# Optimization experiments

Hardware: AMD Instinct MI355X
Metric: run time of the kernel (lower is better)

The kernel has to match this reference:

```python
import jax, jax.numpy as jnp
import numpy as np

NUM_LAYERS = 6
KS = 5  # kernel_size; also attention window size K
EPS_IN = 1e-5  # torch InstanceNorm1d default eps


def _conv1d(x, w, b, d, p):
    # x: [N,C,L], w: [O,I,KS], dilated 'same' conv
    y = jax.lax.conv_general_dilated(x, w, window_strides=(1,), padding=[(p, p)],
                                     rhs_dilation=(d,), dimension_numbers=('NCH', 'OIH', 'NCH'))
    return y + b[None, :, None]


def _pw(x, w, b):
    # pointwise (1x1) conv: x [N,C,L], w [O,C]
    return jnp.einsum('oc,ncl->nol', w, x) + b[None, :, None]


def _layer(x, x_cross, pr, d):
    C, L = x.shape[1], x.shape[2]
    p = (KS // 2) * d  # padding
    conv_w, conv_b, qw, qb, kw, kb, vw, vb, f1w, f1b, f2w, f2b = pr
    out1 = _conv1d(x, conv_w, conv_b, d, p)
    xc = jnp.concatenate([x, x_cross], axis=1)
    q = _pw(xc, qw, qb)            # [N,C,L]
    k = _pw(xc, kw, kb)
    v = _pw(x, vw, vb)
    kp = jnp.pad(k, ((0, 0), (0, 0), (p, p)))
    vp = jnp.pad(v, ((0, 0), (0, 0), (p, p)))
    # attn index for query q, slot j is (q + j*d) into padded axis -> shifted slices
    win_k = jnp.stack([kp[:, :, j * d:j * d + L] for j in range(KS)], axis=-1)  # [N,C,L,K]
    win_v = jnp.stack([vp[:, :, j * d:j * d + L] for j in range(KS)], axis=-1)
    att = jnp.einsum('ncl,nclk->nlk', q, win_k) / np.float32(np.sqrt(C))
    pos = jnp.arange(L)[:, None] + (jnp.arange(KS)[None, :] - KS // 2) * d  # absolute key pos
    mask = (pos >= 0) & (pos < L)  # [L,K]
    att = jax.nn.softmax(att + jnp.log(mask + 1e-6), axis=-1) * mask
    r = jnp.einsum('nlk,nclk->ncl', att, win_v)
    h = out1 + r
    # InstanceNorm1d (no affine): normalize over L per (n,c)
    mu = jnp.mean(h, axis=2, keepdims=True)
    var = jnp.var(h, axis=2, keepdims=True)
    h = (h - mu) * jax.lax.rsqrt(var + EPS_IN)
    out = _pw(jax.nn.relu(_pw(h, f1w, f1b)), f2w, f2b)
    return x + out


def reference(x, x_cross, time_emb, time_w, time_b, conv_w, conv_b, qw, qb, kw, kb, vw, vb, f1w, f1b, f2w, f2b):
    te = time_emb * jax.nn.sigmoid(time_emb)  # swish
    x = x + (te @ time_w.T + time_b)[:, :, None]
    for i in range(NUM_LAYERS):
        pr = (conv_w[i], conv_b[i], qw[i], qb[i], kw[i], kb[i], vw[i], vb[i],
              f1w[i], f1b[i], f2w[i], f2b[i])
        x = _layer(x, x_cross, pr, 2 ** i)
    return x


def setup_inputs() -> dict:
    N, C, CC, L, T, nL = 4, 256, 256, 4096, 512, NUM_LAYERS
    key = jax.random.key(0)
    ks = jax.random.split(key, 18)
    s = 0.05
    return {
        'x': jax.random.normal(ks[0], (N, C, L), jnp.float32),
        'x_cross': jax.random.normal(ks[1], (N, CC, L), jnp.float32),
        'time_emb': jax.random.normal(ks[2], (N, T), jnp.float32),
        'time_w': jax.random.normal(ks[3], (C, T), jnp.float32) * s,
        'time_b': jax.random.normal(ks[4], (C,), jnp.float32) * s,
        'conv_w': jax.random.normal(ks[5], (nL, C, C, KS), jnp.float32) * s,
        'conv_b': jax.random.normal(ks[6], (nL, C), jnp.float32) * s,
        'qw': jax.random.normal(ks[7], (nL, C, C + CC), jnp.float32) * s,
        'qb': jax.random.normal(ks[8], (nL, C), jnp.float32) * s,
        'kw': jax.random.normal(ks[9], (nL, C, C + CC), jnp.float32) * s,
        'kb': jax.random.normal(ks[10], (nL, C), jnp.float32) * s,
        'vw': jax.random.normal(ks[11], (nL, C, C), jnp.float32) * s,
        'vb': jax.random.normal(ks[12], (nL, C), jnp.float32) * s,
        'f1w': jax.random.normal(ks[13], (nL, C, C), jnp.float32) * s,
        'f1b': jax.random.normal(ks[14], (nL, C), jnp.float32) * s,
        'f2w': jax.random.normal(ks[15], (nL, C, C), jnp.float32) * s,
        'f2b': jax.random.normal(ks[16], (nL, C), jnp.float32) * s,
    }
```

## Files before the change

### kernel.cpp

```cpp
#include <hip/hip_runtime.h>
#include <hip/hip_bf16.h>
#include <cstddef>
#include <cstdint>

#define N_   4
#define C_   256
#define L_   4096
#define T_   512
#define KS_  5
#define NL_  6
#define HALO 64
#define LP_  (L_ + 2 * HALO)
#define XCS  512
#define NCH  256

typedef __attribute__((ext_vector_type(8))) __bf16 bf16x8;
typedef __attribute__((ext_vector_type(4))) float f32x4;

#define VM_WAIT3 asm volatile("s_waitcnt vmcnt(3)" ::: "memory")
#define VM_WAIT2 asm volatile("s_waitcnt vmcnt(2)" ::: "memory")
#define VM_WAIT0 asm volatile("s_waitcnt vmcnt(0)" ::: "memory")

__device__ __forceinline__ void gload_lds16(const void* g, void* l) {
    __builtin_amdgcn_global_load_lds(
        (const __attribute__((address_space(1))) unsigned int*)g,
        (__attribute__((address_space(3))) unsigned int*)l, 16, 0, 0);
}
__device__ __forceinline__ float bf2f(unsigned short u) {
    union { unsigned int i; float f; } x; x.i = ((unsigned int)u) << 16; return x.f;
}
__device__ __forceinline__ unsigned short f2bf(float f) {
    __hip_bfloat16 h = __float2bfloat16(f);
    return *reinterpret_cast<unsigned short*>(&h);
}
__device__ __forceinline__ float4 ld4bf(const unsigned short* p) {
    ushort4 u = *reinterpret_cast<const ushort4*>(p);
    return make_float4(bf2f(u.x), bf2f(u.y), bf2f(u.z), bf2f(u.w));
}
__device__ __forceinline__ int swz(int row, int seg) { return seg ^ ((row >> 1) & 3); }

__device__ __forceinline__ void mfma16(bf16x8 af[4], bf16x8 bfr[4], f32x4 acc[4][4])
{
    #pragma unroll
    for (int m = 0; m < 4; m++)
        #pragma unroll
        for (int nn = 0; nn < 4; nn++)
            acc[m][nn] = __builtin_amdgcn_mfma_f32_16x16x32_bf16(af[m], bfr[nn], acc[m][nn], 0, 0, 0);
}

__global__ __launch_bounds__(512) void gemm_cq(
    const unsigned short* __restrict__ xcat,
    const unsigned short* __restrict__ wqkv, const float* __restrict__ qkvbias,
    const unsigned short* __restrict__ wconv, const float* __restrict__ cbias,
    unsigned short* __restrict__ qkvb, unsigned short* __restrict__ convb, int d)
{
    __shared__ alignas(16) unsigned short As[3][256 * 32];
    __shared__ alignas(16) unsigned short Bs[3][128 * 32];
    const int tid = threadIdx.x, wid = tid >> 6, lane = tid & 63;
    const int wr = wid >> 1, wc = wid & 1;
    const int r0 = blockIdx.x * 256;
    const int n = r0 >> 12, lb = r0 & (L_ - 1);
    const int ob = blockIdx.y;
    const bool isconv = (ob < 2);
    f32x4 acc[4][4] = {};
    const int orow = (lane >> 4) * 4, ocol = lane & 15;
    const int rsel = lane & 15, j = lane >> 4;

    auto read_frags = [&](const unsigned short* A, const unsigned short* B,
                          bf16x8 af[4], bf16x8 bfr[4]) {
        #pragma unroll
        for (int m = 0; m < 4; m++) {
            const int r = wr * 64 + m * 16 + rsel;
            af[m] = *reinterpret_cast<const bf16x8*>(&A[r * 32 + swz(r, j) * 8]);
        }
        #pragma unroll
        for (int nn = 0; nn < 4; nn++) {
            const int r = wc * 64 + nn * 16 + rsel;
            bfr[nn] = *reinterpret_cast<const bf16x8*>(&B[r * 32 + swz(r, j) * 8]);
        }
    };

    if (isconv) {
        const int o0 = ob * 128;
        auto stage = [&](int t, int b) {
            const int tap = t >> 3, kb = (t & 7) * 32;
            const size_t abase = (size_t)((long)n * LP_ + HALO + lb + (tap - 2) * d) * XCS;
            const unsigned short* Wj = wconv + (size_t)tap * C_ * C_;
            #pragma unroll
            for (int i = 0; i < 2; i++) {
                const int s = tid + i * 512, row = s >> 2, seg = s & 3;
                gload_lds16(xcat + abase + (size_t)row * XCS + kb + swz(row, seg) * 8,
                            As[b] + s * 8);
            }
            {
                const int row = tid >> 2, seg = tid & 3;
                gload_lds16(Wj + (size_t)(o0 + row) * C_ + kb + swz(row, seg) * 8,
                            Bs[b] + tid * 8);
            }
        };
        const int NT = 40;
        stage(0, 0); stage(1, 1);
        VM_WAIT3;
        __builtin_amdgcn_s_barrier();
        for (int t = 0; t < NT; t++) {
            const int cur = t % 3;
            bf16x8 af[4], bfr[4];
            read_frags(As[cur], Bs[cur], af, bfr);
            if (t + 2 < NT) stage(t + 2, (t + 2) % 3);
            mfma16(af, bfr, acc);
            if (t + 2 < NT) { VM_WAIT3; } else { VM_WAIT0; }
            __builtin_amdgcn_s_barrier();
        }
        #pragma unroll
        for (int m = 0; m < 4; m++)
            #pragma unroll
            for (int nn = 0; nn < 4; nn++) {
                const int gr0 = r0 + wr * 64 + m * 16 + orow;
                const int gc = o0 + wc * 64 + nn * 16 + ocol;
                const float bv = cbias[gc];
                #pragma unroll
                for (int rr = 0; rr < 4; rr++)
                    convb[(size_t)(gr0 + rr) * C_ + gc] = f2bf(acc[m][nn][rr] + bv);
            }
    } else {
        const int o0 = (ob - 2) * 128;
        const size_t abase = ((size_t)n * LP_ + HALO + lb) * XCS;
        auto stage = [&](int t, int b) {
            const int kb = t * 32;
            #pragma unroll
            for (int i = 0; i < 2; i++) {
                const int s = tid + i * 512, row = s >> 2, seg = s & 3;
                gload_lds16(xcat + abase + (size_t)row * XCS + kb + swz(row, seg) * 8,
                            As[b] + s * 8);
            }
            {
                const int row = tid >> 2, seg = tid & 3;
                gload_lds16(wqkv + (size_t)(o0 + row) * 512 + kb + swz(row, seg) * 8,
                            Bs[b] + tid * 8);
            }
        };
        const int NT = (o0 >= 512) ? 8 : 16;
        stage(0, 0); stage(1, 1);
        VM_WAIT3;
        __builtin_amdgcn_s_barrier();
        for (int t = 0; t < NT; t++) {
            const int cur = t % 3;
            bf16x8 af[4], bfr[4];
            read_frags(As[cur], Bs[cur], af, bfr);
            if (t + 2 < NT) stage(t + 2, (t + 2) % 3);
            mfma16(af, bfr, acc);
            if (t + 2 < NT) { VM_WAIT3; } else { VM_WAIT0; }
            __builtin_amdgcn_s_barrier();
        }
        #pragma unroll
        for (int m = 0; m < 4; m++)
            #pragma unroll
            for (int nn = 0; nn < 4; nn++) {
                const int gr0 = r0 + wr * 64 + m * 16 + orow;
                const int gc = o0 + wc * 64 + nn * 16 + ocol;
                const float bv = qkvbias[gc];
                #pragma unroll
                for (int rr = 0; rr < 4; rr++)
                    qkvb[(size_t)(gr0 + rr) * 768 + gc] = f2bf(acc[m][nn][rr] + bv);
            }
    }
}

template <int EP, int PERN>
__global__ __launch_bounds__(256) void gemm_f(
    const unsigned short* __restrict__ A,
    const unsigned short* __restrict__ B,
    const float* __restrict__ bias,
    unsigned short* __restrict__ outb,
    unsigned short* __restrict__ xcat)
{
    __shared__ alignas(16) unsigned short As[3][64 * 32];
    __shared__ alignas(16) unsigned short Bs[3][64 * 32];
    const int tid = threadIdx.x, wid = tid >> 6, lane = tid & 63;
    const int r0 = blockIdx.x * 64;
    const int o0 = blockIdx.y * 64;
    const int n = r0 >> 12;
    if (PERN) {
        B += (size_t)n * C_ * C_;
        bias += n * C_;
    }
    const size_t abase = (size_t)r0 * C_;
    const int rsel = lane & 15, j = lane >> 4;
    f32x4 acc[4] = {};
    auto stage = [&](int t, int b) {
        const int kb = t * 32;
        const int row = tid >> 2, seg = tid & 3;
        const int gso = swz(row, seg) * 8;
        gload_lds16(A + abase + (size_t)row * C_ + kb + gso, As[b] + tid * 8);
        gload_lds16(B + (size_t)(o0 + row) * C_ + kb + gso, Bs[b] + tid * 8);
    };
    const int NT = 8;
    stage(0, 0); stage(1, 1);
    VM_WAIT2;
    __builtin_amdgcn_s_barrier();
    for (int t = 0; t < NT; t++) {
        const int cur = t % 3;
        bf16x8 af, bfr[4];
        {
            const int r = wid * 16 + rsel;
            af = *reinterpret_cast<const bf16x8*>(&As[cur][r * 32 + swz(r, j) * 8]);
        }
        #pragma unroll
        for (int nn = 0; nn < 4; nn++) {
            const int r = nn * 16 + rsel;
            bfr[nn] = *reinterpret_cast<const bf16x8*>(&Bs[cur][r * 32 + swz(r, j) * 8]);
        }
        if (t + 2 < NT) stage(t + 2, (t + 2) % 3);
        #pragma unroll
        for (int nn = 0; nn < 4; nn++)
            acc[nn] = __builtin_amdgcn_mfma_f32_16x16x32_bf16(af, bfr[nn], acc[nn], 0, 0, 0);
        if (t + 2 < NT) { VM_WAIT2; } else { VM_WAIT0; }
        __builtin_amdgcn_s_barrier();
    }
    const int orow = (lane >> 4) * 4, ocol = lane & 15;
    #pragma unroll
    for (int nn = 0; nn < 4; nn++) {
        const int gr0 = r0 + wid * 16 + orow;
        const int gc = o0 + nn * 16 + ocol;
        const float bv = bias[gc];
        #pragma unroll
        for (int rr = 0; rr < 4; rr++) {
            const int gr = gr0 + rr;
            const float v = acc[nn][rr] + bv;
            if (EP == 2) {
                outb[(size_t)gr * C_ + gc] = f2bf(fmaxf(v, 0.f));
            } else {
                const int n2 = gr >> 12, ll = gr & (L_ - 1);
                unsigned short* xp = xcat + ((size_t)n2 * LP_ + HALO + ll) * XCS + gc;
                *xp = f2bf(v + bf2f(*xp));
            }
        }
    }
}

__global__ __launch_bounds__(256) void attn_fused(
    const unsigned short* __restrict__ qkv, const unsigned short* __restrict__ convb,
    unsigned short* __restrict__ hb2, float* __restrict__ psum, float* __restrict__ psq, int d)
{
    __shared__ float ps[4][256], pq[4][256];
    const int n = blockIdx.y;
    const int wave = threadIdx.x >> 6;
    const int lane = threadIdx.x & 63;
    float acs[4] = {0.f, 0.f, 0.f, 0.f}, acq[4] = {0.f, 0.f, 0.f, 0.f};
    for (int lq = 0; lq < 4; lq++) {
        const int l = blockIdx.x * 16 + wave * 4 + lq;
        const float4 qv = ld4bf(qkv + ((size_t)n * L_ + l) * 768 + lane * 4);
        float att[KS_];
        #pragma unroll
        for (int j = 0; j < KS_; j++) {
            const int lp = l + (j - 2) * d;
            float s = 0.f;
            if (lp >= 0 && lp < L_) {
                const float4 kv = ld4bf(qkv + ((size_t)n * L_ + lp) * 768 + 256 + lane * 4);
                s = qv.x * kv.x + qv.y * kv.y + qv.z * kv.z + qv.w * kv.w;
            }
            #pragma unroll
            for (int off = 32; off > 0; off >>= 1) s += __shfl_xor(s, off, 64);
            att[j] = s * 0.0625f;
        }
        float logit[KS_], m = -1e30f;
        #pragma unroll
        for (int j = 0; j < KS_; j++) {
            const int lp = l + (j - 2) * d;
            logit[j] = att[j] + logf(((lp >= 0 && lp < L_) ? 1.f : 0.f) + 1e-6f);
            m = fmaxf(m, logit[j]);
        }
        float den = 0.f, wgt[KS_];
        #pragma unroll
        for (int j = 0; j < KS_; j++) { wgt[j] = expf(logit[j] - m); den += wgt[j]; }
        const float inv = 1.f / den;
        float4 r = {0.f, 0.f, 0.f, 0.f};
        #pragma unroll
        for (int j = 0; j < KS_; j++) {
            const int lp = l + (j - 2) * d;
            if (lp < 0 || lp >= L_) continue;
            const float wj = wgt[j] * inv;
            const float4 vv = ld4bf(qkv + ((size_t)n * L_ + lp) * 768 + 512 + lane * 4);
            r.x += wj * vv.x; r.y += wj * vv.y; r.z += wj * vv.z; r.w += wj * vv.w;
        }
        const size_t rowoff = ((size_t)n * L_ + l) * C_ + lane * 4;
        const float4 cv = ld4bf(convb + rowoff);
        const float h0 = cv.x + r.x, h1 = cv.y + r.y, h2 = cv.z + r.z, h3 = cv.w + r.w;
        ushort4 ho;
        ho.x = f2bf(h0); ho.y = f2bf(h1); ho.z = f2bf(h2); ho.w = f2bf(h3);
        *(ushort4*)(hb2 + rowoff) = ho;
        acs[0] += h0; acs[1] += h1; acs[2] += h2; acs[3] += h3;
        acq[0] += h0 * h0; acq[1] += h1 * h1; acq[2] += h2 * h2; acq[3] += h3 * h3;
    }
    const int cb4 = lane * 4;
    #pragma unroll
    for (int u = 0; u < 4; u++) { ps[wave][cb4 + u] = acs[u]; pq[wave][cb4 + u] = acq[u]; }
    __syncthreads();
    const int t = threadIdx.x;
    psum[((size_t)n * NCH + blockIdx.x) * C_ + t] = ps[0][t] + ps[1][t] + ps[2][t] + ps[3][t];
    psq[((size_t)n * NCH + blockIdx.x) * C_ + t] = pq[0][t] + pq[1][t] + pq[2][t] + pq[3][t];
}

__global__ __launch_bounds__(256) void norm_red(
    const float* __restrict__ psum, const float* __restrict__ psq,
    float* __restrict__ psum2, float* __restrict__ psq2)
{
    const int g = blockIdx.x, n = blockIdx.y, c = threadIdx.x;
    float s = 0.f, ss = 0.f;
    for (int ch = g * 16; ch < g * 16 + 16; ch++) {
        s += psum[((size_t)n * NCH + ch) * C_ + c];
        ss += psq[((size_t)n * NCH + ch) * C_ + c];
    }
    psum2[((size_t)n * 16 + g) * C_ + c] = s;
    psq2[((size_t)n * 16 + g) * C_ + c] = ss;
}

__global__ __launch_bounds__(256) void fold_f1(
    const float* __restrict__ f1w, const float* __restrict__ f1b,
    const float* __restrict__ psum2, const float* __restrict__ psq2,
    unsigned short* __restrict__ W1p, float* __restrict__ b1eff)
{
    const int b = blockIdx.x;
    const int n = b >> 8, o = b & 255;
    const int c = threadIdx.x;
    const int lane = c & 63, wid = c >> 6;
    float s = 0.f, ss = 0.f;
    #pragma unroll
    for (int g = 0; g < 16; g++) {
        s += psum2[((size_t)n * 16 + g) * C_ + c];
        ss += psq2[((size_t)n * 16 + g) * C_ + c];
    }
    const float mu = s * (1.f / L_);
    const float scv = rsqrtf(ss * (1.f / L_) - mu * mu + 1e-5f);
    const float w = f1w[o * C_ + c];
    W1p[((size_t)n * C_ + o) * C_ + c] = f2bf(w * scv);
    float part = w * mu * scv;
    #pragma unroll
    for (int off = 32; off > 0; off >>= 1) part += __shfl_xor(part, off, 64);
    __shared__ float red[4];
    if (lane == 0) red[wid] = part;
    __syncthreads();
    if (c == 0) b1eff[n * C_ + o] = f1b[o] - (red[0] + red[1] + red[2] + red[3]);
}

__global__ __launch_bounds__(128) void time_bias_kernel(
    const float* __restrict__ te, const float* __restrict__ tw,
    const float* __restrict__ tb, float* __restrict__ bias)
{
    int nc = blockIdx.x;
    int n = nc >> 8, c = nc & 255;
    int tid = threadIdx.x;
    float s = 0.f;
    for (int t = tid; t < T_; t += 128) {
        float e = te[n * T_ + t];
        s += (e / (1.f + expf(-e))) * tw[c * T_ + t];
    }
    __shared__ float red[128];
    red[tid] = s;
    __syncthreads();
    for (int off = 64; off > 0; off >>= 1) {
        if (tid < off) red[tid] += red[tid + off];
        __syncthreads();
    }
    if (tid == 0) bias[nc] = red[0] + tb[c];
}

__global__ __launch_bounds__(256) void halo_zero(unsigned short* __restrict__ xcat)
{
    const int t = blockIdx.x * 256 + threadIdx.x;
    const int n = t >> 14, rr = (t >> 7) & 127, c4 = t & 127;
    const int row = (rr < 64) ? rr : (L_ + HALO) + (rr - 64);
    ushort4 z = {0, 0, 0, 0};
    *(ushort4*)(xcat + ((size_t)n * LP_ + row) * XCS + c4 * 4) = z;
}

template <int MODE>
__global__ __launch_bounds__(256) void transpose_in(
    const float* __restrict__ in, const float* __restrict__ bias,
    unsigned short* __restrict__ xcat)
{
    __shared__ float tile[32][33];
    const int n = blockIdx.z;
    const int l0 = blockIdx.x * 32, c0 = blockIdx.y * 32;
    const int tx = threadIdx.x, ty = threadIdx.y;
    #pragma unroll
    for (int i = 0; i < 4; i++) {
        int c = c0 + ty + 8 * i;
        tile[ty + 8 * i][tx] = in[((size_t)n * C_ + c) * L_ + l0 + tx];
    }
    __syncthreads();
    #pragma unroll
    for (int i = 0; i < 4; i++) {
        const int l = l0 + ty + 8 * i;
        const int c = c0 + tx;
        float v = tile[tx][ty + 8 * i];
        if (MODE == 0) {
            v += bias[n * C_ + c];
            xcat[((size_t)n * LP_ + HALO + l) * XCS + c] = f2bf(v);
        } else {
            xcat[((size_t)n * LP_ + HALO + l) * XCS + C_ + c] = f2bf(v);
        }
    }
}

__global__ __launch_bounds__(256) void transpose_out(
    const unsigned short* __restrict__ xcat, float* __restrict__ out)
{
    __shared__ float tile[32][33];
    const int n = blockIdx.z;
    const int l0 = blockIdx.x * 32, c0 = blockIdx.y * 32;
    const int tx = threadIdx.x, ty = threadIdx.y;
    #pragma unroll
    for (int i = 0; i < 4; i++) {
        int l = l0 + ty + 8 * i;
        tile[ty + 8 * i][tx] = bf2f(xcat[((size_t)n * LP_ + HALO + l) * XCS + c0 + tx]);
    }
    __syncthreads();
    #pragma unroll
    for (int i = 0; i < 4; i++) {
        int c = c0 + ty + 8 * i;
        out[((size_t)n * C_ + c) * L_ + l0 + tx] = tile[tx][ty + 8 * i];
    }
}

__global__ __launch_bounds__(256) void prep_qkv(
    const float* __restrict__ qw, const float* __restrict__ kw, const float* __restrict__ vw,
    const float* __restrict__ qb, const float* __restrict__ kb, const float* __restrict__ vb,
    unsigned short* __restrict__ W, float* __restrict__ Bias)
{
    const size_t idx = (size_t)blockIdx.x * 256 + threadIdx.x;
    const int layer = (int)(idx / (768 * 512));
    const int rem = (int)(idx % (768 * 512));
    const int row = rem >> 9, k = rem & 511;
    float v;
    if (row < 256) v = qw[((size_t)layer * 256 + row) * 512 + k];
    else if (row < 512) v = kw[((size_t)layer * 256 + row - 256) * 512 + k];
    else v = (k < 256) ? vw[((size_t)layer * 256 + row - 512) * 256 + k] : 0.f;
    W[idx] = f2bf(v);
    if (k == 0) {
        float b;
        if (row < 256) b = qb[layer * 256 + row];
        else if (row < 512) b = kb[layer * 256 + row - 256];
        else b = vb[layer * 256 + row - 512];
        Bias[layer * 768 + row] = b;
    }
}

__global__ __launch_bounds__(256) void prep_conv(
    const float* __restrict__ cw, unsigned short* __restrict__ W)
{
    const size_t idx = (size_t)blockIdx.x * 256 + threadIdx.x;
    const int layer = (int)(idx / (KS_ * C_ * C_));
    const int rem = (int)(idx % (KS_ * C_ * C_));
    const int j = rem / (C_ * C_);
    const int o = (rem / C_) & 255, c = rem & 255;
    W[idx] = f2bf(cw[(((size_t)layer * C_ + o) * C_ + c) * KS_ + j]);
}

__global__ __launch_bounds__(256) void conv_f2bf(
    const float* __restrict__ in, unsigned short* __restrict__ out, int nelem)
{
    const int idx = blockIdx.x * 256 + threadIdx.x;
    if (idx < nelem) out[idx] = f2bf(in[idx]);
}

extern "C" void kernel_launch(void* const* d_in, const int* in_sizes, int n_in,
                              void* d_out, int out_size, void* d_ws, size_t ws_size,
                              hipStream_t stream)
{
    (void)in_sizes; (void)n_in; (void)out_size; (void)ws_size;
    const float* x   = (const float*)d_in[0];
    const float* xc  = (const float*)d_in[1];
    const float* te  = (const float*)d_in[2];
    const float* tw  = (const float*)d_in[3];
    const float* tb  = (const float*)d_in[4];
    const float* cw  = (const float*)d_in[5];
    const float* cb  = (const float*)d_in[6];
    const float* qw  = (const float*)d_in[7];
    const float* qbi = (const float*)d_in[8];
    const float* kw  = (const float*)d_in[9];
    const float* kbi = (const float*)d_in[10];
    const float* vw  = (const float*)d_in[11];
    const float* vbi = (const float*)d_in[12];
    const float* f1w = (const float*)d_in[13];
    const float* f1b = (const float*)d_in[14];
    const float* f2w = (const float*)d_in[15];
    const float* f2b = (const float*)d_in[16];

    char* p = (char*)d_ws;
    auto alloc = [&](size_t bytes) { char* r = p; p += (bytes + 255) & ~(size_t)255; return r; };
    const size_t NLC = (size_t)N_ * L_ * C_;
    unsigned short* xcat  = (unsigned short*)alloc((size_t)N_ * LP_ * XCS * 2);
    unsigned short* qkvb  = (unsigned short*)alloc((size_t)N_ * L_ * 768 * 2);
    unsigned short* convb = (unsigned short*)alloc(NLC * 2);
    unsigned short* hb2   = (unsigned short*)alloc(NLC * 2);
    unsigned short* f1ob  = (unsigned short*)alloc(NLC * 2);
    unsigned short* wqkvb = (unsigned short*)alloc((size_t)NL_ * 768 * 512 * 2);
    unsigned short* wconvb= (unsigned short*)alloc((size_t)NL_ * KS_ * C_ * C_ * 2);
    unsigned short* wf2b  = (unsigned short*)alloc((size_t)NL_ * C_ * C_ * 2);
    unsigned short* W1p   = (unsigned short*)alloc((size_t)N_ * C_ * C_ * 2);
    float* b1eff  = (float*)alloc((size_t)N_ * C_ * 4);
    float* qkvbias = (float*)alloc((size_t)NL_ * 768 * 4);
    float* biasb = (float*)alloc(N_ * C_ * 4);
    float* psum  = (float*)alloc((size_t)N_ * NCH * C_ * 4);
    float* psq   = (float*)alloc((size_t)N_ * NCH * C_ * 4);
    float* psum2 = (float*)alloc((size_t)N_ * 16 * C_ * 4);
    float* psq2  = (float*)alloc((size_t)N_ * 16 * C_ * 4);

    halo_zero<<<256, 256, 0, stream>>>(xcat);
    prep_qkv<<<(NL_ * 768 * 512) / 256, 256, 0, stream>>>(qw, kw, vw, qbi, kbi, vbi, wqkvb, qkvbias);
    prep_conv<<<(NL_ * KS_ * C_ * C_) / 256, 256, 0, stream>>>(cw, wconvb);
    conv_f2bf<<<(NL_ * C_ * C_) / 256, 256, 0, stream>>>(f2w, wf2b, NL_ * C_ * C_);

    time_bias_kernel<<<N_ * C_, 128, 0, stream>>>(te, tw, tb, biasb);
    dim3 tgrid(L_ / 32, C_ / 32, N_), tblk(32, 8);
    transpose_in<0><<<tgrid, tblk, 0, stream>>>(x, biasb, xcat);
    transpose_in<1><<<tgrid, tblk, 0, stream>>>(xc, nullptr, xcat);

    for (int i = 0; i < NL_; i++) {
        const int d = 1 << i;
        gemm_cq<<<dim3(64, 8), 512, 0, stream>>>(
            xcat, wqkvb + (size_t)i * 768 * 512, qkvbias + i * 768,
            wconvb + (size_t)i * KS_ * C_ * C_, cb + i * C_, qkvb, convb, d);
        attn_fused<<<dim3(L_ / 16, N_), 256, 0, stream>>>(qkvb, convb, hb2, psum, psq, d);
        norm_red<<<dim3(16, N_), 256, 0, stream>>>(psum, psq, psum2, psq2);
        fold_f1<<<N_ * C_, 256, 0, stream>>>(
            f1w + (size_t)i * C_ * C_, f1b + i * C_, psum2, psq2, W1p, b1eff);
        gemm_f<2, 1><<<dim3(256, 4), 256, 0, stream>>>(
            hb2, W1p, b1eff, f1ob, nullptr);
        gemm_f<3, 0><<<dim3(256, 4), 256, 0, stream>>>(
            f1ob, wf2b + (size_t)i * C_ * C_, f2b + i * C_, nullptr, xcat);
    }
    transpose_out<<<tgrid, tblk, 0, stream>>>(xcat, (float*)d_out);
}
```

Measured before the change: 476.3 us.

## Recast dilated conv as per-tap pointwise GEMM columns summed in attention

Packs the five conv taps as extra output columns of a single unified GEMM with Q/K/V, so every GEMM block runs the same short K loop over unshifted rows. The attention kernel then gathers and sums the tap outputs at the dilated neighbor positions, alongside K and V, and adds the conv bias. This removes the long 40-step conv blocks and their load imbalance, but writes and rereads a much wider intermediate buffer per layer.

After: 497.2 us. 1.04x slower.

```diff
diff --git a/kernel.cpp b/kernel.cpp
--- a/kernel.cpp
+++ b/kernel.cpp
@@ -12,6 +12,7 @@
 #define HALO 64
 #define LP_  (L_ + 2 * HALO)
 #define XCS  512
+#define OBS  2048
 #define NCH  256
 
 typedef __attribute__((ext_vector_type(8))) __bf16 bf16x8;
@@ -48,11 +49,10 @@
             acc[m][nn] = __builtin_amdgcn_mfma_f32_16x16x32_bf16(af[m], bfr[nn], acc[m][nn], 0, 0, 0);
 }
 
-__global__ __launch_bounds__(512) void gemm_cq(
+__global__ __launch_bounds__(512) void gemm_all(
     const unsigned short* __restrict__ xcat,
-    const unsigned short* __restrict__ wqkv, const float* __restrict__ qkvbias,
-    const unsigned short* __restrict__ wconv, const float* __restrict__ cbias,
-    unsigned short* __restrict__ qkvb, unsigned short* __restrict__ convb, int d)
+    const unsigned short* __restrict__ wpack, const float* __restrict__ pbias,
+    unsigned short* __restrict__ obuf)
 {
     __shared__ alignas(16) unsigned short As[3][256 * 32];
     __shared__ alignas(16) unsigned short Bs[3][128 * 32];
@@ -60,110 +60,59 @@
     const int wr = wid >> 1, wc = wid & 1;
     const int r0 = blockIdx.x * 256;
     const int n = r0 >> 12, lb = r0 & (L_ - 1);
-    const int ob = blockIdx.y;
-    const bool isconv = (ob < 2);
+    const int o0 = blockIdx.y * 128;
+    const int NT = (blockIdx.y < 4) ? 16 : 8;
+    const size_t abase = ((size_t)n * LP_ + HALO + lb) * XCS;
     f32x4 acc[4][4] = {};
     const int orow = (lane >> 4) * 4, ocol = lane & 15;
     const int rsel = lane & 15, j = lane >> 4;
 
-    auto read_frags = [&](const unsigned short* A, const unsigned short* B,
-                          bf16x8 af[4], bf16x8 bfr[4]) {
+    auto stage = [&](int t, int b) {
+        const int kb = t * 32;
+        #pragma unroll
+        for (int i = 0; i < 2; i++) {
+            const int s = tid + i * 512, row = s >> 2, seg = s & 3;
+            gload_lds16(xcat + abase + (size_t)row * XCS + kb + swz(row, seg) * 8,
+                        As[b] + s * 8);
+        }
+        {
+            const int row = tid >> 2, seg = tid & 3;
+            gload_lds16(wpack + (size_t)(o0 + row) * 512 + kb + swz(row, seg) * 8,
+                        Bs[b] + tid * 8);
+        }
+    };
+    stage(0, 0); stage(1, 1);
+    VM_WAIT3;
+    __builtin_amdgcn_s_barrier();
+    for (int t = 0; t < NT; t++) {
+        const int cur = t % 3;
+        bf16x8 af[4], bfr[4];
         #pragma unroll
         for (int m = 0; m < 4; m++) {
             const int r = wr * 64 + m * 16 + rsel;
-            af[m] = *reinterpret_cast<const bf16x8*>(&A[r * 32 + swz(r, j) * 8]);
+            af[m] = *reinterpret_cast<const bf16x8*>(&As[cur][r * 32 + swz(r, j) * 8]);
         }
         #pragma unroll
         for (int nn = 0; nn < 4; nn++) {
             const int r = wc * 64 + nn * 16 + rsel;
-            bfr[nn] = *reinterpret_cast<const bf16x8*>(&B[r * 32 + swz(r, j) * 8]);
-        }
-    };
-
-    if (isconv) {
-        const int o0 = ob * 128;
-        auto stage = [&](int t, int b) {
-            const int tap = t >> 3, kb = (t & 7) * 32;
-            const size_t abase = (size_t)((long)n * LP_ + HALO + lb + (tap - 2) * d) * XCS;
-            const unsigned short* Wj = wconv + (size_t)tap * C_ * C_;
+            bfr[nn] = *reinterpret_cast<const bf16x8*>(&Bs[cur][r * 32 + swz(r, j) * 8]);
+        }
+        if (t + 2 < NT) stage(t + 2, (t + 2) % 3);
+        mfma16(af, bfr, acc);
+        if (t + 2 < NT) { VM_WAIT3; } else { VM_WAIT0; }
+        __builtin_amdgcn_s_barrier();
+    }
+    #pragma unroll
+    for (int m = 0; m < 4; m++)
+        #pragma unroll
+        for (int nn = 0; nn < 4; nn++) {
+            const int gr0 = r0 + wr * 64 + m * 16 + orow;
+            const int gc = o0 + wc * 64 + nn * 16 + ocol;
+            const float bv = pbias[gc];
             #pragma unroll
-            for (int i = 0; i < 2; i++) {
-                const int s = tid + i * 512, row = s >> 2, seg = s & 3;
-                gload_lds16(xcat + abase + (size_t)row * XCS + kb + swz(row, seg) * 8,
-                            As[b] + s * 8);
-            }
-            {
-                const int row = tid >> 2, seg = tid & 3;
-                gload_lds16(Wj + (size_t)(o0 + row) * C_ + kb + swz(row, seg) * 8,
-                            Bs[b] + tid * 8);
-            }
-        };
-        const int NT = 40;
-        stage(0, 0); stage(1, 1);
-        VM_WAIT3;
-        __builtin_amdgcn_s_barrier();
-        for (int t = 0; t < NT; t++) {
-            const int cur = t % 3;
-            bf16x8 af[4], bfr[4];
-            read_frags(As[cur], Bs[cur], af, bfr);
-            if (t + 2 < NT) stage(t + 2, (t + 2) % 3);
-            mfma16(af, bfr, acc);
-            if (t + 2 < NT) { VM_WAIT3; } else { VM_WAIT0; }
-            __builtin_amdgcn_s_barrier();
-        }
-        #pragma unroll
-        for (int m = 0; m < 4; m++)
-            #pragma unroll
-            for (int nn = 0; nn < 4; nn++) {
-                const int gr0 = r0 + wr * 64 + m * 16 + orow;
-                const int gc = o0 + wc * 64 + nn * 16 + ocol;
-                const float bv = cbias[gc];
-                #pragma unroll
-                for (int rr = 0; rr < 4; rr++)
-                    convb[(size_t)(gr0 + rr) * C_ + gc] = f2bf(acc[m][nn][rr] + bv);
-            }
-    } else {
-        const int o0 = (ob - 2) * 128;
-        const size_t abase = ((size_t)n * LP_ + HALO + lb) * XCS;
-        auto stage = [&](int t, int b) {
-            const int kb = t * 32;
-            #pragma unroll
-            for (int i = 0; i < 2; i++) {
-                const int s = tid + i * 512, row = s >> 2, seg = s & 3;
-                gload_lds16(xcat + abase + (size_t)row * XCS + kb + swz(row, seg) * 8,
-                            As[b] + s * 8);
-            }
-            {
-                const int row = tid >> 2, seg = tid & 3;
-                gload_lds16(wqkv + (size_t)(o0 + row) * 512 + kb + swz(row, seg) * 8,
-                            Bs[b] + tid * 8);
-            }
-        };
-        const int NT = (o0 >= 512) ? 8 : 16;
-        stage(0, 0); stage(1, 1);
-        VM_WAIT3;
-        __builtin_amdgcn_s_barrier();
-        for (int t = 0; t < NT; t++) {
-            const int cur = t % 3;
-            bf16x8 af[4], bfr[4];
-            read_frags(As[cur], Bs[cur], af, bfr);
-            if (t + 2 < NT) stage(t + 2, (t + 2) % 3);
-            mfma16(af, bfr, acc);
-            if (t + 2 < NT) { VM_WAIT3; } else { VM_WAIT0; }
-            __builtin_amdgcn_s_barrier();
-        }
-        #pragma unroll
-        for (int m = 0; m < 4; m++)
-            #pragma unroll
-            for (int nn = 0; nn < 4; nn++) {
-                const int gr0 = r0 + wr * 64 + m * 16 + orow;
-                const int gc = o0 + wc * 64 + nn * 16 + ocol;
-                const float bv = qkvbias[gc];
-                #pragma unroll
-                for (int rr = 0; rr < 4; rr++)
-                    qkvb[(size_t)(gr0 + rr) * 768 + gc] = f2bf(acc[m][nn][rr] + bv);
-            }
-    }
+            for (int rr = 0; rr < 4; rr++)
+                obuf[(size_t)(gr0 + rr) * OBS + gc] = f2bf(acc[m][nn][rr] + bv);
+        }
 }
 
 template <int EP, int PERN>
@@ -239,25 +188,31 @@
 }
 
 __global__ __launch_bounds__(256) void attn_fused(
-    const unsigned short* __restrict__ qkv, const unsigned short* __restrict__ convb,
+    const unsigned short* __restrict__ obuf, const float* __restrict__ cbias,
     unsigned short* __restrict__ hb2, float* __restrict__ psum, float* __restrict__ psq, int d)
 {
     __shared__ float ps[4][256], pq[4][256];
     const int n = blockIdx.y;
     const int wave = threadIdx.x >> 6;
     const int lane = threadIdx.x & 63;
+    const float4 cb = *(const float4*)(cbias + lane * 4);
     float acs[4] = {0.f, 0.f, 0.f, 0.f}, acq[4] = {0.f, 0.f, 0.f, 0.f};
     for (int lq = 0; lq < 4; lq++) {
         const int l = blockIdx.x * 16 + wave * 4 + lq;
-        const float4 qv = ld4bf(qkv + ((size_t)n * L_ + l) * 768 + lane * 4);
+        const size_t rb = ((size_t)n * L_ + l) * OBS;
+        const float4 qv = ld4bf(obuf + rb + lane * 4);
         float att[KS_];
+        float4 cv = {0.f, 0.f, 0.f, 0.f};
         #pragma unroll
         for (int j = 0; j < KS_; j++) {
             const int lp = l + (j - 2) * d;
             float s = 0.f;
             if (lp >= 0 && lp < L_) {
-                const float4 kv = ld4bf(qkv + ((size_t)n * L_ + lp) * 768 + 256 + lane * 4);
+                const size_t rp = ((size_t)n * L_ + lp) * OBS;
+                const float4 kv = ld4bf(obuf + rp + 256 + lane * 4);
                 s = qv.x * kv.x + qv.y * kv.y + qv.z * kv.z + qv.w * kv.w;
+                const float4 tv = ld4bf(obuf + rp + 768 + j * 256 + lane * 4);
+                cv.x += tv.x; cv.y += tv.y; cv.z += tv.z; cv.w += tv.w;
             }
             #pragma unroll
             for (int off = 32; off > 0; off >>= 1) s += __shfl_xor(s, off, 64);
@@ -280,12 +235,12 @@
             const int lp = l + (j - 2) * d;
             if (lp < 0 || lp >= L_) continue;
             const float wj = wgt[j] * inv;
-            const float4 vv = ld4bf(qkv + ((size_t)n * L_ + lp) * 768 + 512 + lane * 4);
+            const float4 vv = ld4bf(obuf + ((size_t)n * L_ + lp) * OBS + 512 + lane * 4);
             r.x += wj * vv.x; r.y += wj * vv.y; r.z += wj * vv.z; r.w += wj * vv.w;
         }
+        const float h0 = cv.x + cb.x + r.x, h1 = cv.y + cb.y + r.y;
+        const float h2 = cv.z + cb.z + r.z, h3 = cv.w + cb.w + r.w;
         const size_t rowoff = ((size_t)n * L_ + l) * C_ + lane * 4;
-        const float4 cv = ld4bf(convb + rowoff);
-        const float h0 = cv.x + r.x, h1 = cv.y + r.y, h2 = cv.z + r.z, h3 = cv.w + r.w;
         ushort4 ho;
         ho.x = f2bf(h0); ho.y = f2bf(h1); ho.z = f2bf(h2); ho.w = f2bf(h3);
         *(ushort4*)(hb2 + rowoff) = ho;
@@ -423,38 +378,32 @@
     }
 }
 
-__global__ __launch_bounds__(256) void prep_qkv(
-    const float* __restrict__ qw, const float* __restrict__ kw, const float* __restrict__ vw,
+__global__ __launch_bounds__(256) void prep_pack(
+    const float* __restrict__ qw, const float* __restrict__ kw,
+    const float* __restrict__ vw, const float* __restrict__ cw,
     const float* __restrict__ qb, const float* __restrict__ kb, const float* __restrict__ vb,
-    unsigned short* __restrict__ W, float* __restrict__ Bias)
+    unsigned short* __restrict__ wpack, float* __restrict__ pbias)
 {
     const size_t idx = (size_t)blockIdx.x * 256 + threadIdx.x;
-    const int layer = (int)(idx / (768 * 512));
-    const int rem = (int)(idx % (768 * 512));
+    const int layer = (int)(idx / (2048 * 512));
+    const int rem = (int)(idx % (2048 * 512));
     const int row = rem >> 9, k = rem & 511;
     float v;
     if (row < 256) v = qw[((size_t)layer * 256 + row) * 512 + k];
     else if (row < 512) v = kw[((size_t)layer * 256 + row - 256) * 512 + k];
-    else v = (k < 256) ? vw[((size_t)layer * 256 + row - 512) * 256 + k] : 0.f;
-    W[idx] = f2bf(v);
+    else if (row < 768) v = (k < 256) ? vw[((size_t)layer * 256 + row - 512) * 256 + k] : 0.f;
+    else {
+        const int tj = (row - 768) >> 8, o = (row - 768) & 255;
+        v = (k < 256) ? cw[(((size_t)layer * 256 + o) * 256 + k) * KS_ + tj] : 0.f;
+    }
+    wpack[idx] = f2bf(v);
     if (k == 0) {
-        float b;
+        float b = 0.f;
         if (row < 256) b = qb[layer * 256 + row];
         else if (row < 512) b = kb[layer * 256 + row - 256];
-        else b = vb[layer * 256 + row - 512];
-        Bias[layer * 768 + row] = b;
-    }
-}
-
-__global__ __launch_bounds__(256) void prep_conv(
-    const float* __restrict__ cw, unsigned short* __restrict__ W)
-{
-    const size_t idx = (size_t)blockIdx.x * 256 + threadIdx.x;
-    const int layer = (int)(idx / (KS_ * C_ * C_));
-    const int rem = (int)(idx % (KS_ * C_ * C_));
-    const int j = rem / (C_ * C_);
-    const int o = (rem / C_) & 255, c = rem & 255;
-    W[idx] = f2bf(cw[(((size_t)layer * C_ + o) * C_ + c) * KS_ + j]);
+        else if (row < 768) b = vb[layer * 256 + row - 512];
+        pbias[layer * 2048 + row] = b;
+    }
 }
 
 __global__ __launch_bounds__(256) void conv_f2bf(
@@ -491,25 +440,23 @@
     auto alloc = [&](size_t bytes) { char* r = p; p += (bytes + 255) & ~(size_t)255; return r; };
     const size_t NLC = (size_t)N_ * L_ * C_;
     unsigned short* xcat  = (unsigned short*)alloc((size_t)N_ * LP_ * XCS * 2);
-    unsigned short* qkvb  = (unsigned short*)alloc((size_t)N_ * L_ * 768 * 2);
-    unsigned short* convb = (unsigned short*)alloc(NLC * 2);
+    unsigned short* obuf  = (unsigned short*)alloc((size_t)N_ * L_ * OBS * 2);
     unsigned short* hb2   = (unsigned short*)alloc(NLC * 2);
-    unsigned short* f1ob  = (unsigned short*)alloc(NLC * 2);
-    unsigned short* wqkvb = (unsigned short*)alloc((size_t)NL_ * 768 * 512 * 2);
-    unsigned short* wconvb= (unsigned short*)alloc((size_t)NL_ * KS_ * C_ * C_ * 2);
+    unsigned short* wpack = (unsigned short*)alloc((size_t)NL_ * 2048 * 512 * 2);
     unsigned short* wf2b  = (unsigned short*)alloc((size_t)NL_ * C_ * C_ * 2);
     unsigned short* W1p   = (unsigned short*)alloc((size_t)N_ * C_ * C_ * 2);
     float* b1eff  = (float*)alloc((size_t)N_ * C_ * 4);
-    float* qkvbias = (float*)alloc((size_t)NL_ * 768 * 4);
-    float* biasb = (float*)alloc(N_ * C_ * 4);
-    float* psum  = (float*)alloc((size_t)N_ * NCH * C_ * 4);
-    float* psq   = (float*)alloc((size_t)N_ * NCH * C_ * 4);
-    float* psum2 = (float*)alloc((size_t)N_ * 16 * C_ * 4);
-    float* psq2  = (float*)alloc((size_t)N_ * 16 * C_ * 4);
+    float* pbias  = (float*)alloc((size_t)NL_ * 2048 * 4);
+    float* biasb  = (float*)alloc(N_ * C_ * 4);
+    float* psum   = (float*)alloc((size_t)N_ * NCH * C_ * 4);
+    float* psq    = (float*)alloc((size_t)N_ * NCH * C_ * 4);
+    float* psum2  = (float*)alloc((size_t)N_ * 16 * C_ * 4);
+    float* psq2   = (float*)alloc((size_t)N_ * 16 * C_ * 4);
+    unsigned short* f1ob = obuf;
 
     halo_zero<<<256, 256, 0, stream>>>(xcat);
-    prep_qkv<<<(NL_ * 768 * 512) / 256, 256, 0, stream>>>(qw, kw, vw, qbi, kbi, vbi, wqkvb, qkvbias);
-    prep_conv<<<(NL_ * KS_ * C_ * C_) / 256, 256, 0, stream>>>(cw, wconvb);
+    prep_pack<<<(NL_ * 2048 * 512) / 256, 256, 0, stream>>>(
+        qw, kw, vw, cw, qbi, kbi, vbi, wpack, pbias);
     conv_f2bf<<<(NL_ * C_ * C_) / 256, 256, 0, stream>>>(f2w, wf2b, NL_ * C_ * C_);
 
     time_bias_kernel<<<N_ * C_, 128, 0, stream>>>(te, tw, tb, biasb);
@@ -519,10 +466,10 @@
 
     for (int i = 0; i < NL_; i++) {
         const int d = 1 << i;
-        gemm_cq<<<dim3(64, 8), 512, 0, stream>>>(
-            xcat, wqkvb + (size_t)i * 768 * 512, qkvbias + i * 768,
-            wconvb + (size_t)i * KS_ * C_ * C_, cb + i * C_, qkvb, convb, d);
-        attn_fused<<<dim3(L_ / 16, N_), 256, 0, stream>>>(qkvb, convb, hb2, psum, psq, d);
+        gemm_all<<<dim3(64, 16), 512, 0, stream>>>(
+            xcat, wpack + (size_t)i * 2048 * 512, pbias + i * 2048, obuf);
+        attn_fused<<<dim3(L_ / 16, N_), 256, 0, stream>>>(
+            obuf, cb + i * C_, hb2, psum, psq, d);
         norm_red<<<dim3(16, N_), 256, 0, stream>>>(psum, psq, psum2, psq2);
         fold_f1<<<N_ * C_, 256, 0, stream>>>(
             f1w + (size_t)i * C_ * C_, f1b + i * C_, psum2, psq2, W1p, b1eff);
```
